# Performance work log

Hardware: AMD Instinct MI355X
Metric: run time of the kernel (lower is better)

Reference implementation:

```python
import jax, jax.numpy as jnp
import numpy as np

NB_OBJ = 16
BATCH = 64
F_IN = 32768
HID = 64
N_AGENTS = 4
N_ACT = 13
NEG_SLOPE = 0.01  # torch LeakyReLU default


def _build_edges():
    # fully connected minus diagonal, per graph; GCNConv adds self-loops
    adj = np.ones((NB_OBJ, NB_OBJ)) - np.eye(NB_OBJ)
    r, c = np.nonzero(adj)
    loop = np.arange(NB_OBJ)
    src = np.concatenate([r, loop])
    dst = np.concatenate([c, loop])
    offs = (np.arange(BATCH) * NB_OBJ)[:, None]
    src_all = (src[None, :] + offs).reshape(-1)
    dst_all = (dst[None, :] + offs).reshape(-1)
    return jnp.asarray(src_all, jnp.int32), jnp.asarray(dst_all, jnp.int32)


def setup_inputs() -> dict:
    key = jax.random.key(0)
    ks = jax.random.split(key, 9)
    s = 1.0 / np.sqrt(F_IN)
    sh = 1.0 / np.sqrt(HID)
    return {
        "unary_tensor": jax.random.normal(ks[0], (BATCH, NB_OBJ, F_IN), jnp.float32),
        "binary_tensor": jax.random.uniform(ks[1], (BATCH, NB_OBJ, NB_OBJ, 2), jnp.float32),
        "actions": jax.random.normal(ks[2], (N_AGENTS, BATCH, N_ACT), jnp.float32),
        "gcn_w": jax.random.uniform(ks[3], (F_IN, HID), jnp.float32, -s, s),
        "gcn_b": jax.random.uniform(ks[4], (HID,), jnp.float32, -s, s),
        "head_w1": jax.random.uniform(ks[5], (N_AGENTS, HID, HID), jnp.float32, -sh, sh),
        "head_b1": jax.random.uniform(ks[6], (N_AGENTS, HID), jnp.float32, -sh, sh),
        "head_w2": jax.random.uniform(ks[7], (N_AGENTS, HID, N_ACT), jnp.float32, -sh, sh),
        "head_b2": jax.random.uniform(ks[8], (N_AGENTS, N_ACT), jnp.float32, -sh, sh),
    }


def reference(unary_tensor, binary_tensor, actions, gcn_w, gcn_b,
              head_w1, head_b1, head_w2, head_b2):
    src, dst = _build_edges()
    x = unary_tensor.reshape(BATCH * NB_OBJ, F_IN)  # flatten(0,1)
    lin = x @ gcn_w  # [1024, HID]
    # GCN symmetric norm: every node has degree 16 (15 neighbors + self loop)
    norm = 1.0 / NB_OBJ
    msg = lin[src] * norm
    agg = jax.ops.segment_sum(msg, dst, num_segments=BATCH * NB_OBJ)
    h = agg + gcn_b  # [1024, HID]
    # split into graphs and max-pool over nodes
    pooled = jnp.max(h.reshape(BATCH, NB_OBJ, HID), axis=1)  # [64, HID]
    # per-agent critic heads
    z = jnp.einsum('bh,ahk->abk', pooled, head_w1) + head_b1[:, None, :]
    z = jnp.where(z >= 0, z, NEG_SLOPE * z)  # LeakyReLU
    all_q = jnp.einsum('abh,ahk->abk', z, head_w2) + head_b2[:, None, :]  # [A,64,13]
    int_acs = jnp.argmax(actions, axis=2)  # [A, 64]
    q = jnp.take_along_axis(all_q, int_acs[:, :, None], axis=2)  # [A, 64, 1]
    return q
```

## Files before the change

kernel.cpp:

```cpp
#include <hip/hip_runtime.h>

#define F_IN    32768
#define HID     64
#define NB_OBJ  16
#define BATCH   64
#define N_AGENTS 4
#define N_ACT   13
#define NEG_SLOPE 0.01f

#define FC      64
#define NCHUNK  (F_IN / FC)
#define BH      32

typedef float f32x4 __attribute__((ext_vector_type(4)));

__device__ float g_part[NCHUNK * BATCH * HID];

__global__ __launch_bounds__(256, 4)
void k_gcn_partial(const float* __restrict__ u, const float* __restrict__ w) {
    __shared__ float xbar[BH][FC + 4];
    const int t     = threadIdx.x;
    const int blk   = blockIdx.x >> 1;
    const int bhalf = blockIdx.x & 1;
    const int f0    = blk * FC;
    const int b0    = bhalf * BH;
    const int lane  = t & 63;
    const int wv    = t >> 6;

    float wreg[FC];
    {
        const float* wp = w + (size_t)f0 * HID + lane;
        #pragma unroll
        for (int f = 0; f < FC; ++f) wreg[f] = wp[f * HID];
    }

    {
        const int b = t >> 3;
        const int j = t & 7;
        const float* up = u + (size_t)(b0 + b) * (NB_OBJ * F_IN) + f0 + j * 4;
        f32x4 a0 = (f32x4)(0.f);
        f32x4 a1 = (f32x4)(0.f);
        #pragma unroll
        for (int o = 0; o < NB_OBJ; ++o) {
            const float* ro = up + o * F_IN;
            f32x4 v0 = __builtin_nontemporal_load(reinterpret_cast<const f32x4*>(ro));
            f32x4 v1 = __builtin_nontemporal_load(reinterpret_cast<const f32x4*>(ro + 32));
            a0 += v0;
            a1 += v1;
        }
        const float inv = 1.0f / (float)NB_OBJ;
        a0 *= inv;
        a1 *= inv;
        *reinterpret_cast<f32x4*>(&xbar[b][j * 4])      = a0;
        *reinterpret_cast<f32x4*>(&xbar[b][32 + j * 4]) = a1;
    }
    __syncthreads();

    {
        float* pout = g_part + (size_t)blk * (BATCH * HID) + (size_t)b0 * HID + lane;
        #pragma unroll
        for (int bb = 0; bb < 8; ++bb) {
            const int b = wv * 8 + bb;
            float acc = 0.f;
            #pragma unroll
            for (int fq = 0; fq < FC / 4; ++fq) {
                f32x4 xb = *reinterpret_cast<const f32x4*>(&xbar[b][fq * 4]);
                acc += xb.x * wreg[fq * 4 + 0];
                acc += xb.y * wreg[fq * 4 + 1];
                acc += xb.z * wreg[fq * 4 + 2];
                acc += xb.w * wreg[fq * 4 + 3];
            }
            pout[b * HID] = acc;
        }
    }
}

__global__ __launch_bounds__(512)
void k_tail(const float* __restrict__ gcn_b,
            const float* __restrict__ w1, const float* __restrict__ b1,
            const float* __restrict__ w2, const float* __restrict__ b2,
            const float* __restrict__ actions, float* __restrict__ out) {
    const int b = blockIdx.x;
    const int t = threadIdx.x;
    __shared__ float red[8][HID];
    __shared__ float pooled[HID];
    __shared__ float zbuf[N_AGENTS][HID];
    __shared__ float qbuf[N_AGENTS][N_ACT];

    {
        const int h  = t & 63;
        const int kg = t >> 6;
        const float* p = g_part + (size_t)(kg * 64) * (BATCH * HID)
                       + (size_t)b * HID + h;
        float acc = 0.f;
        #pragma unroll 16
        for (int i = 0; i < 64; ++i)
            acc += p[(size_t)i * (BATCH * HID)];
        red[kg][h] = acc;
    }
    __syncthreads();
    if (t < HID) {
        float acc = gcn_b[t];
        #pragma unroll
        for (int kg = 0; kg < 8; ++kg) acc += red[kg][t];
        pooled[t] = acc;
    }
    __syncthreads();

    if (t < N_AGENTS * HID) {
        const int a = t >> 6, k = t & 63;
        const float* w1p = w1 + a * (HID * HID) + k;
        float acc = b1[a * HID + k];
        #pragma unroll
        for (int hh = 0; hh < HID; ++hh) acc += pooled[hh] * w1p[hh * HID];
        zbuf[a][k] = (acc >= 0.f) ? acc : NEG_SLOPE * acc;
    }
    __syncthreads();

    if (t < N_AGENTS * N_ACT) {
        const int a = t / N_ACT, c = t % N_ACT;
        const float* w2p = w2 + a * (HID * N_ACT) + c;
        float acc = b2[a * N_ACT + c];
        #pragma unroll
        for (int hh = 0; hh < HID; ++hh) acc += zbuf[a][hh] * w2p[hh * N_ACT];
        qbuf[a][c] = acc;
    }
    __syncthreads();

    if (t < N_AGENTS) {
        const float* ap = actions + ((size_t)t * BATCH + b) * N_ACT;
        int best = 0; float bv = ap[0];
        for (int c = 1; c < N_ACT; ++c) {
            float v = ap[c];
            if (v > bv) { bv = v; best = c; }
        }
        out[t * BATCH + b] = qbuf[t][best];
    }
}

extern "C" void kernel_launch(void* const* d_in, const int* in_sizes, int n_in,
                              void* d_out, int out_size, void* d_ws, size_t ws_size,
                              hipStream_t stream) {
    const float* u   = (const float*)d_in[0];
    const float* act = (const float*)d_in[2];
    const float* gw  = (const float*)d_in[3];
    const float* gb  = (const float*)d_in[4];
    const float* w1  = (const float*)d_in[5];
    const float* b1  = (const float*)d_in[6];
    const float* w2  = (const float*)d_in[7];
    const float* b2  = (const float*)d_in[8];
    float* out = (float*)d_out;

    hipLaunchKernelGGL(k_gcn_partial, dim3(NCHUNK * 2), dim3(256), 0, stream, u, gw);
    hipLaunchKernelGGL(k_tail,        dim3(BATCH),      dim3(512), 0, stream,
                       gb, w1, b1, w2, b2, act, out);
}
```

Before: 40.32 us.

## Split node-mean reduction into separate kernel before GCN GEMM

Unfusion: the per-graph node mean is moved out of the partial GEMM into its own streaming kernel that writes an intermediate [64, 32768] buffer to global memory. The GEMM kernel then loads that buffer for all 64 batch rows per feature chunk, which halves the block count and loads each weight slice once instead of twice. The goal is a simpler, fully coalesced streaming pass over the 128 MB input. The cost is an extra kernel launch and an 8 MB intermediate write and read, plus dropping the nontemporal load hints.

New measurement: 46.73 us. +15.9%, slower.

```diff
diff --git a/kernel.cpp b/kernel.cpp
--- a/kernel.cpp
+++ b/kernel.cpp
@@ -10,22 +10,48 @@
 
 #define FC      64
 #define NCHUNK  (F_IN / FC)
-#define BH      32
 
 typedef float f32x4 __attribute__((ext_vector_type(4)));
 
+__device__ float g_s[BATCH * F_IN];
 __device__ float g_part[NCHUNK * BATCH * HID];
 
 __global__ __launch_bounds__(256, 4)
-void k_gcn_partial(const float* __restrict__ u, const float* __restrict__ w) {
-    __shared__ float xbar[BH][FC + 4];
-    const int t     = threadIdx.x;
-    const int blk   = blockIdx.x >> 1;
-    const int bhalf = blockIdx.x & 1;
-    const int f0    = blk * FC;
-    const int b0    = bhalf * BH;
-    const int lane  = t & 63;
-    const int wv    = t >> 6;
+void k_mean(const float* __restrict__ u) {
+    const int t   = threadIdx.x;
+    const int bid = blockIdx.x;
+    const int b   = bid >> 5;
+    const int fq  = (bid & 31) * 256 + t;
+    const float* base = u + (size_t)b * (NB_OBJ * F_IN) + (size_t)fq * 4;
+
+    f32x4 a0 = (f32x4)(0.f), a1 = (f32x4)(0.f);
+    #pragma unroll
+    for (int o = 0; o < NB_OBJ; o += 2) {
+        a0 += *reinterpret_cast<const f32x4*>(base + (size_t)o * F_IN);
+        a1 += *reinterpret_cast<const f32x4*>(base + (size_t)(o + 1) * F_IN);
+    }
+    f32x4 s = (a0 + a1) * (1.0f / (float)NB_OBJ);
+    *reinterpret_cast<f32x4*>(g_s + (size_t)b * F_IN + (size_t)fq * 4) = s;
+}
+
+__global__ __launch_bounds__(256, 4)
+void k_gemm(const float* __restrict__ w) {
+    __shared__ float xbar[BATCH][FC + 4];
+    const int t    = threadIdx.x;
+    const int blk  = blockIdx.x;
+    const int f0   = blk * FC;
+    const int lane = t & 63;
+    const int wv   = t >> 6;
+
+    {
+        const int b = t >> 2, j = t & 3;
+        const float* sp = g_s + (size_t)b * F_IN + f0;
+        #pragma unroll
+        for (int q = 0; q < 4; ++q) {
+            f32x4 v = *reinterpret_cast<const f32x4*>(sp + (j + 4 * q) * 4);
+            *reinterpret_cast<f32x4*>(&xbar[b][(j + 4 * q) * 4]) = v;
+        }
+    }
 
     float wreg[FC];
     {
@@ -33,34 +59,13 @@
         #pragma unroll
         for (int f = 0; f < FC; ++f) wreg[f] = wp[f * HID];
     }
-
-    {
-        const int b = t >> 3;
-        const int j = t & 7;
-        const float* up = u + (size_t)(b0 + b) * (NB_OBJ * F_IN) + f0 + j * 4;
-        f32x4 a0 = (f32x4)(0.f);
-        f32x4 a1 = (f32x4)(0.f);
-        #pragma unroll
-        for (int o = 0; o < NB_OBJ; ++o) {
-            const float* ro = up + o * F_IN;
-            f32x4 v0 = __builtin_nontemporal_load(reinterpret_cast<const f32x4*>(ro));
-            f32x4 v1 = __builtin_nontemporal_load(reinterpret_cast<const f32x4*>(ro + 32));
-            a0 += v0;
-            a1 += v1;
-        }
-        const float inv = 1.0f / (float)NB_OBJ;
-        a0 *= inv;
-        a1 *= inv;
-        *reinterpret_cast<f32x4*>(&xbar[b][j * 4])      = a0;
-        *reinterpret_cast<f32x4*>(&xbar[b][32 + j * 4]) = a1;
-    }
     __syncthreads();
 
     {
-        float* pout = g_part + (size_t)blk * (BATCH * HID) + (size_t)b0 * HID + lane;
+        float* pout = g_part + (size_t)blk * (BATCH * HID) + lane;
         #pragma unroll
-        for (int bb = 0; bb < 8; ++bb) {
-            const int b = wv * 8 + bb;
+        for (int bb = 0; bb < 16; ++bb) {
+            const int b = wv * 16 + bb;
             float acc = 0.f;
             #pragma unroll
             for (int fq = 0; fq < FC / 4; ++fq) {
@@ -151,7 +156,8 @@
     const float* b2  = (const float*)d_in[8];
     float* out = (float*)d_out;
 
-    hipLaunchKernelGGL(k_gcn_partial, dim3(NCHUNK * 2), dim3(256), 0, stream, u, gw);
-    hipLaunchKernelGGL(k_tail,        dim3(BATCH),      dim3(512), 0, stream,
+    hipLaunchKernelGGL(k_mean, dim3(2048),   dim3(256), 0, stream, u);
+    hipLaunchKernelGGL(k_gemm, dim3(NCHUNK), dim3(256), 0, stream, gw);
+    hipLaunchKernelGGL(k_tail, dim3(BATCH),  dim3(512), 0, stream,
                        gb, w1, b1, w2, b2, act, out);
 }
```
